# Optimization experiments

Measured on AMD Instinct MI355X. Metric: run time of the kernel, lower is better.

## Reference

```python
import jax, jax.numpy as jnp
import numpy as np

N_NODES = 100000


def _gcn_conv(x, edge_index, W, b, n_nodes):
    """PyG GCNConv: add self-loops, symmetric deg^-1/2 normalization,
    linear transform, scatter-sum aggregation, bias."""
    loop = jnp.arange(n_nodes, dtype=edge_index.dtype)
    src = jnp.concatenate([edge_index[0], loop])  # message sources
    dst = jnp.concatenate([edge_index[1], loop])  # message targets
    deg = jax.ops.segment_sum(jnp.ones_like(dst, dtype=x.dtype), dst,
                              num_segments=n_nodes)
    dinv = jnp.where(deg > 0, jax.lax.rsqrt(jnp.maximum(deg, 1.0)), 0.0)
    norm = dinv[src] * dinv[dst]  # [E+N]
    h = x @ W  # [N, out] transform before aggregation (fewer bytes moved)
    msg = h[src] * norm[:, None]  # [E+N, out]
    out = jax.ops.segment_sum(msg, dst, num_segments=n_nodes)
    return out + b


def setup_inputs() -> dict:
    key = jax.random.key(0)
    k1, k2, k3, k4, k5, k6 = jax.random.split(key, 6)
    in_ch, hid, out_ch = 128, 64, 64
    x = jax.random.normal(k1, (N_NODES, in_ch), dtype=jnp.float32)
    edge_index = jax.random.randint(k2, (2, 3200000), 0, N_NODES, dtype=jnp.int64)
    # Glorot-style init for GCN weights, zeros for bias (PyG default)
    W1 = jax.random.normal(k3, (in_ch, hid), dtype=jnp.float32) / np.sqrt(in_ch)
    b1 = jnp.zeros((hid,), dtype=jnp.float32)
    W2 = jax.random.normal(k4, (hid, out_ch), dtype=jnp.float32) / np.sqrt(hid)
    b2 = jnp.zeros((out_ch,), dtype=jnp.float32)
    return {"x": x, "edge_index": edge_index, "W1": W1, "b1": b1,
            "W2": W2, "b2": b2}


def reference(x, edge_index, W1, b1, W2, b2):
    n = x.shape[0]
    h = _gcn_conv(x, edge_index, W1, b1, n)
    h = jax.nn.relu(h)
    out = _gcn_conv(h, edge_index, W2, b2, n)
    return out
```

## Files before the change

kernel.cpp:

```cpp
#include <hip/hip_runtime.h>
#include <math.h>


#define BKT_SHIFT 9
#define BKT_NODES 512
#define NBSH      256
#define CHUNK     8192
#define MAXB      20480

typedef unsigned short ushort_t;
typedef _Float16 h2_t __attribute__((ext_vector_type(2)));
typedef _Float16 h4_t __attribute__((ext_vector_type(4)));

__global__ __launch_bounds__(256) void bucket_bin(const int* __restrict__ src,
                                                  const int* __restrict__ dst,
                                                  int* __restrict__ bcur,
                                                  unsigned* __restrict__ pairs,
                                                  int E, int NB) {
    __shared__ unsigned stag[CHUNK];
    __shared__ int hist[NBSH];
    __shared__ int lofs[NBSH];
    __shared__ int lcur[NBSH];
    __shared__ int gbase[NBSH];
    const int t  = threadIdx.x;
    const int e0 = blockIdx.x * CHUNK;
    const int n  = min(CHUNK, E - e0);

    for (int i = t; i < NBSH; i += 256) hist[i] = 0;
    __syncthreads();
    for (int i = t; i < n; i += 256) atomicAdd(&hist[dst[e0 + i] >> BKT_SHIFT], 1);
    __syncthreads();
    int v = hist[t];
    lofs[t] = v;
    __syncthreads();
    for (int d = 1; d < 256; d <<= 1) {
        int u = (t >= d) ? lofs[t - d] : 0;
        __syncthreads();
        lofs[t] += u;
        __syncthreads();
    }
    if (t < NB) {
        lcur[t]  = lofs[t] - v;
        gbase[t] = (v > 0) ? t * MAXB + atomicAdd(&bcur[t], v) : 0;
    }
    __syncthreads();
    for (int i = t; i < n; i += 256) {
        int d = dst[e0 + i];
        int s = src[e0 + i];
        int b = d >> BKT_SHIFT;
        int p = atomicAdd(&lcur[b], 1);
        stag[p] = ((unsigned)(d & (BKT_NODES - 1)) << 17) | (unsigned)s;
    }
    __syncthreads();
    const int wv = t >> 6, ln = t & 63;
    for (int b = wv; b < NB; b += 4) {
        int cb = hist[b];
        if (cb == 0) continue;
        int lo = lofs[b] - cb;
        int gb = gbase[b];
        int lim = min(cb, (b + 1) * MAXB - gb);
        for (int i = ln; i < lim; i += 64) pairs[gb + i] = stag[lo + i];
    }
}

__global__ __launch_bounds__(1024) void csr_sort(const unsigned* __restrict__ pairs,
                                                 const int* __restrict__ bcur,
                                                 unsigned* __restrict__ csr,
                                                 int* __restrict__ cnt,
                                                 int* __restrict__ offs,
                                                 float* __restrict__ dinv, int N) {
    extern __shared__ unsigned st[];
    __shared__ int h[BKT_NODES];
    __shared__ int sc[BKT_NODES];
    __shared__ int cur[BKT_NODES];
    const int b    = blockIdx.x;
    const int t    = threadIdx.x;
    const int n0   = b << BKT_SHIFT;
    const int base = b * MAXB;
    const int ne   = min(bcur[b], MAXB);

    if (t < BKT_NODES) h[t] = 0;
    __syncthreads();
    for (int i = t; i < ne; i += 1024) atomicAdd(&h[pairs[base + i] >> 17], 1);
    __syncthreads();
    int v = 0;
    if (t < BKT_NODES) { v = h[t]; sc[t] = v; }
    __syncthreads();
    for (int d = 1; d < BKT_NODES; d <<= 1) {
        int u = (t < BKT_NODES && t >= d) ? sc[t - d] : 0;
        __syncthreads();
        if (t < BKT_NODES) sc[t] += u;
        __syncthreads();
    }
    if (t < BKT_NODES) {
        int ex = sc[t] - v;
        cur[t] = ex;
        int node = n0 + t;
        if (node < N) {
            cnt[node]  = v;
            offs[node] = base + ex;
            dinv[node] = rsqrtf((float)(v + 1));
        }
    }
    __syncthreads();
    for (int i = t; i < ne; i += 1024) {
        unsigned p = pairs[base + i];
        int pos = atomicAdd(&cur[p >> 17], 1);
        st[pos] = p & 0x1FFFFu;
    }
    __syncthreads();
    for (int i = t; i < ne; i += 1024) csr[base + i] = st[i];
}

template <int K>
__global__ __launch_bounds__(256) void gemm_scale(const float* __restrict__ X,
                                                  const float* __restrict__ W,
                                                  const float* __restrict__ dinv,
                                                  ushort_t* __restrict__ G, int N) {
    __shared__ float Ws[K * 64];
    const int t  = threadIdx.x;
    const int r0 = blockIdx.x * 128;

    for (int i = t; i < K * 16; i += 256)
        ((float4*)Ws)[i] = ((const float4*)W)[i];

    const int cg = (t & 15) * 4;
    const int rb = r0 + (t >> 4) * 8;

    float acc[8][4];
#pragma unroll
    for (int j = 0; j < 8; ++j) {
        acc[j][0] = 0.f; acc[j][1] = 0.f; acc[j][2] = 0.f; acc[j][3] = 0.f;
    }
    __syncthreads();

    const bool full = (rb + 8 <= N);
    for (int k = 0; k < K; k += 4) {
        float4 xr[8];
        if (full) {
#pragma unroll
            for (int j = 0; j < 8; ++j)
                xr[j] = *(const float4*)(X + (size_t)(rb + j) * K + k);
        } else {
#pragma unroll
            for (int j = 0; j < 8; ++j)
                xr[j] = (rb + j < N) ? *(const float4*)(X + (size_t)(rb + j) * K + k)
                                     : make_float4(0.f, 0.f, 0.f, 0.f);
        }
#pragma unroll
        for (int kk = 0; kk < 4; ++kk) {
            float4 w = *(const float4*)&Ws[(k + kk) * 64 + cg];
#pragma unroll
            for (int j = 0; j < 8; ++j) {
                float xv = (&xr[j].x)[kk];
                acc[j][0] = fmaf(xv, w.x, acc[j][0]);
                acc[j][1] = fmaf(xv, w.y, acc[j][1]);
                acc[j][2] = fmaf(xv, w.z, acc[j][2]);
                acc[j][3] = fmaf(xv, w.w, acc[j][3]);
            }
        }
    }

#pragma unroll
    for (int j = 0; j < 8; ++j) {
        int row = rb + j;
        if (row < N) {
            float s = dinv[row];
            h4_t o = { (_Float16)(acc[j][0] * s), (_Float16)(acc[j][1] * s),
                       (_Float16)(acc[j][2] * s), (_Float16)(acc[j][3] * s) };
            *(h4_t*)(G + (size_t)row * 64 + cg) = o;
        }
    }
}

#define B2(u) __builtin_bit_cast(h2_t, (u))
#define DOT8(v)                                                          \
    acc[0] = __builtin_amdgcn_fdot2(B2((v).x), selx, acc[0], false);     \
    acc[1] = __builtin_amdgcn_fdot2(B2((v).x), sely, acc[1], false);     \
    acc[2] = __builtin_amdgcn_fdot2(B2((v).y), selx, acc[2], false);     \
    acc[3] = __builtin_amdgcn_fdot2(B2((v).y), sely, acc[3], false);     \
    acc[4] = __builtin_amdgcn_fdot2(B2((v).z), selx, acc[4], false);     \
    acc[5] = __builtin_amdgcn_fdot2(B2((v).z), sely, acc[5], false);     \
    acc[6] = __builtin_amdgcn_fdot2(B2((v).w), selx, acc[6], false);     \
    acc[7] = __builtin_amdgcn_fdot2(B2((v).w), sely, acc[7], false);

__global__ __launch_bounds__(256) void aggregate5(const ushort_t* __restrict__ G,
                                                  const int* __restrict__ offs,
                                                  const int* __restrict__ cnt,
                                                  const unsigned* __restrict__ csr,
                                                  const float* __restrict__ dinv,
                                                  const float* __restrict__ bias,
                                                  float* __restrict__ out, int N,
                                                  int do_relu) {
    int w    = (blockIdx.x * 256 + threadIdx.x) >> 6;
    int lane = threadIdx.x & 63;
    if (w >= N) return;
    const int grp = lane >> 3;
    const int sub = lane & 7;
    const int beg = offs[w];
    const int num = cnt[w];

    const h2_t selx = {(_Float16)1.0f, (_Float16)0.0f};
    const h2_t sely = {(_Float16)0.0f, (_Float16)1.0f};

    float acc[8] = {0.f, 0.f, 0.f, 0.f, 0.f, 0.f, 0.f, 0.f};
    if (grp == 0) {
        uint4 v = *(const uint4*)(G + (size_t)w * 64 + sub * 8);
        DOT8(v);
    }

    int e = 0;
    for (; e + 32 <= num; e += 32) {
        unsigned s0 = csr[beg + e + grp];
        unsigned s1 = csr[beg + e + 8 + grp];
        unsigned s2 = csr[beg + e + 16 + grp];
        unsigned s3 = csr[beg + e + 24 + grp];
        uint4 v0 = *(const uint4*)(G + ((size_t)s0 << 6) + (sub << 3));
        uint4 v1 = *(const uint4*)(G + ((size_t)s1 << 6) + (sub << 3));
        uint4 v2 = *(const uint4*)(G + ((size_t)s2 << 6) + (sub << 3));
        uint4 v3 = *(const uint4*)(G + ((size_t)s3 << 6) + (sub << 3));
        DOT8(v0); DOT8(v1); DOT8(v2); DOT8(v3);
    }
    if (e + 16 <= num) {
        unsigned s0 = csr[beg + e + grp];
        unsigned s1 = csr[beg + e + 8 + grp];
        uint4 v0 = *(const uint4*)(G + ((size_t)s0 << 6) + (sub << 3));
        uint4 v1 = *(const uint4*)(G + ((size_t)s1 << 6) + (sub << 3));
        DOT8(v0); DOT8(v1);
        e += 16;
    }
    if (e + 8 <= num) {
        unsigned s0 = csr[beg + e + grp];
        uint4 v0 = *(const uint4*)(G + ((size_t)s0 << 6) + (sub << 3));
        DOT8(v0);
        e += 8;
    }
    int rem = num - e;
    if (grp < rem) {
        unsigned s0 = csr[beg + e + grp];
        uint4 v0 = *(const uint4*)(G + ((size_t)s0 << 6) + (sub << 3));
        DOT8(v0);
    }

#pragma unroll
    for (int m = 8; m <= 32; m <<= 1) {
#pragma unroll
        for (int j = 0; j < 8; ++j) acc[j] += __shfl_xor(acc[j], m, 64);
    }

    if (grp == 0) {
        float d = dinv[w];
        float4 bl0 = *(const float4*)(bias + sub * 8);
        float4 bl1 = *(const float4*)(bias + sub * 8 + 4);
        float4 o0 = make_float4(fmaf(acc[0], d, bl0.x), fmaf(acc[1], d, bl0.y),
                                fmaf(acc[2], d, bl0.z), fmaf(acc[3], d, bl0.w));
        float4 o1 = make_float4(fmaf(acc[4], d, bl1.x), fmaf(acc[5], d, bl1.y),
                                fmaf(acc[6], d, bl1.z), fmaf(acc[7], d, bl1.w));
        if (do_relu) {
            o0.x = fmaxf(o0.x, 0.f); o0.y = fmaxf(o0.y, 0.f);
            o0.z = fmaxf(o0.z, 0.f); o0.w = fmaxf(o0.w, 0.f);
            o1.x = fmaxf(o1.x, 0.f); o1.y = fmaxf(o1.y, 0.f);
            o1.z = fmaxf(o1.z, 0.f); o1.w = fmaxf(o1.w, 0.f);
        }
        *(float4*)(out + (size_t)w * 64 + sub * 8)     = o0;
        *(float4*)(out + (size_t)w * 64 + sub * 8 + 4) = o1;
    }
}

extern "C" void kernel_launch(void* const* d_in, const int* in_sizes, int n_in,
                              void* d_out, int out_size, void* d_ws, size_t ws_size,
                              hipStream_t stream) {
    const float* x  = (const float*)d_in[0];
    const int*   ei = (const int*)d_in[1];
    const float* W1 = (const float*)d_in[2];
    const float* b1 = (const float*)d_in[3];
    const float* W2 = (const float*)d_in[4];
    const float* b2 = (const float*)d_in[5];
    float* out = (float*)d_out;

    const int IN_CH = 128;
    const int N = in_sizes[0] / IN_CH;
    const int E = in_sizes[1] / 2;
    const int* src = ei;
    const int* dst = ei + E;
    const int NB = (N + BKT_NODES - 1) >> BKT_SHIFT;

    char* ws = (char*)d_ws;
    size_t off = 0;
    auto take = [&](size_t bytes) -> char* {
        char* p = ws + off;
        off += (bytes + 255) & ~(size_t)255;
        return p;
    };
    float*    dinv  = (float*)take((size_t)N * 4);
    int*      cnt   = (int*)take((size_t)N * 4);
    int*      offs  = (int*)take((size_t)N * 4);
    int*      bcur  = (int*)take(NBSH * 4);
    unsigned* csr   = (unsigned*)take(((size_t)NB * MAXB + 64) * 4);
    ushort_t* g     = (ushort_t*)take((size_t)N * 64 * 2);
    float*    a1    = (float*)take((size_t)N * 64 * 4);
    unsigned* pairs = (unsigned*)a1;

    const int nbC = (E + CHUNK - 1) / CHUNK;

    hipMemsetAsync(bcur, 0, NBSH * 4, stream);
    bucket_bin<<<nbC, 256, 0, stream>>>(src, dst, bcur, pairs, E, NB);
    csr_sort<<<NB, 1024, MAXB * 4, stream>>>(pairs, bcur, csr, cnt, offs, dinv, N);

    gemm_scale<128><<<(N + 127) / 128, 256, 0, stream>>>(x, W1, dinv, g, N);
    aggregate5<<<(N + 3) / 4, 256, 0, stream>>>(g, offs, cnt, csr, dinv, b1, a1, N, 1);
    gemm_scale<64><<<(N + 127) / 128, 256, 0, stream>>>(a1, W2, dinv, g, N);
    aggregate5<<<(N + 3) / 4, 256, 0, stream>>>(g, offs, cnt, csr, dinv, b2, out, N, 0);
}
```

Before: 334.8 us.

## Replace bucketed LDS CSR sort with global atomic histogram, scan and scatter

Builds the CSR adjacency with a global per-node histogram using atomics, a three-stage prefix scan, and an atomic scatter of source indices, replacing the two-stage bucket binning and shared-memory sort. Offsets now include a sentinel so the aggregation derives counts from adjacent offsets. This removes the fixed per-bucket capacity and the pairs staging buffer, but relies on millions of contended global atomics and uncoalesced random writes, and adds more kernel launches.

```diff
diff --git a/kernel.cpp b/kernel.cpp
--- a/kernel.cpp
+++ b/kernel.cpp
@@ -1,116 +1,89 @@
 #include <hip/hip_runtime.h>
 #include <math.h>
 
-
-#define BKT_SHIFT 9
-#define BKT_NODES 512
-#define NBSH      256
-#define CHUNK     8192
-#define MAXB      20480
 
 typedef unsigned short ushort_t;
 typedef _Float16 h2_t __attribute__((ext_vector_type(2)));
 typedef _Float16 h4_t __attribute__((ext_vector_type(4)));
 
-__global__ __launch_bounds__(256) void bucket_bin(const int* __restrict__ src,
-                                                  const int* __restrict__ dst,
-                                                  int* __restrict__ bcur,
-                                                  unsigned* __restrict__ pairs,
-                                                  int E, int NB) {
-    __shared__ unsigned stag[CHUNK];
-    __shared__ int hist[NBSH];
-    __shared__ int lofs[NBSH];
-    __shared__ int lcur[NBSH];
-    __shared__ int gbase[NBSH];
-    const int t  = threadIdx.x;
-    const int e0 = blockIdx.x * CHUNK;
-    const int n  = min(CHUNK, E - e0);
-
-    for (int i = t; i < NBSH; i += 256) hist[i] = 0;
-    __syncthreads();
-    for (int i = t; i < n; i += 256) atomicAdd(&hist[dst[e0 + i] >> BKT_SHIFT], 1);
-    __syncthreads();
-    int v = hist[t];
-    lofs[t] = v;
+
+__global__ __launch_bounds__(256) void hist_k(const int* __restrict__ dst,
+                                              int* __restrict__ hist, int E) {
+    int i = blockIdx.x * 256 + threadIdx.x;
+    const int stride = gridDim.x * 256;
+    for (; i < E; i += stride) atomicAdd(&hist[dst[i]], 1);
+}
+
+__global__ __launch_bounds__(256) void scan_blk(const int* __restrict__ hist,
+                                                int* __restrict__ bsum, int N) {
+    __shared__ int sh[256];
+    const int t = threadIdx.x;
+    const int i = blockIdx.x * 256 + t;
+    sh[t] = (i < N) ? hist[i] : 0;
+    __syncthreads();
+    for (int d = 128; d > 0; d >>= 1) {
+        if (t < d) sh[t] += sh[t + d];
+        __syncthreads();
+    }
+    if (t == 0) bsum[blockIdx.x] = sh[0];
+}
+
+__global__ __launch_bounds__(512) void scan_top(const int* __restrict__ bsum,
+                                                int* __restrict__ bbase, int nb) {
+    __shared__ int sh[512];
+    const int t = threadIdx.x;
+    int v = (t < nb) ? bsum[t] : 0;
+    sh[t] = v;
+    __syncthreads();
+    for (int d = 1; d < 512; d <<= 1) {
+        int u = (t >= d) ? sh[t - d] : 0;
+        __syncthreads();
+        sh[t] += u;
+        __syncthreads();
+    }
+    if (t < nb) bbase[t] = sh[t] - v;
+}
+
+__global__ __launch_bounds__(256) void scan_fin(const int* __restrict__ hist,
+                                                const int* __restrict__ bbase,
+                                                int* __restrict__ offs,
+                                                int* __restrict__ cur,
+                                                float* __restrict__ dinv, int N) {
+    __shared__ int sh[256];
+    const int t = threadIdx.x;
+    const int i = blockIdx.x * 256 + t;
+    const int v = (i < N) ? hist[i] : 0;
+    sh[t] = v;
     __syncthreads();
     for (int d = 1; d < 256; d <<= 1) {
-        int u = (t >= d) ? lofs[t - d] : 0;
-        __syncthreads();
-        lofs[t] += u;
-        __syncthreads();
-    }
-    if (t < NB) {
-        lcur[t]  = lofs[t] - v;
-        gbase[t] = (v > 0) ? t * MAXB + atomicAdd(&bcur[t], v) : 0;
-    }
-    __syncthreads();
-    for (int i = t; i < n; i += 256) {
-        int d = dst[e0 + i];
-        int s = src[e0 + i];
-        int b = d >> BKT_SHIFT;
-        int p = atomicAdd(&lcur[b], 1);
-        stag[p] = ((unsigned)(d & (BKT_NODES - 1)) << 17) | (unsigned)s;
-    }
-    __syncthreads();
-    const int wv = t >> 6, ln = t & 63;
-    for (int b = wv; b < NB; b += 4) {
-        int cb = hist[b];
-        if (cb == 0) continue;
-        int lo = lofs[b] - cb;
-        int gb = gbase[b];
-        int lim = min(cb, (b + 1) * MAXB - gb);
-        for (int i = ln; i < lim; i += 64) pairs[gb + i] = stag[lo + i];
-    }
-}
-
-__global__ __launch_bounds__(1024) void csr_sort(const unsigned* __restrict__ pairs,
-                                                 const int* __restrict__ bcur,
-                                                 unsigned* __restrict__ csr,
-                                                 int* __restrict__ cnt,
-                                                 int* __restrict__ offs,
-                                                 float* __restrict__ dinv, int N) {
-    extern __shared__ unsigned st[];
-    __shared__ int h[BKT_NODES];
-    __shared__ int sc[BKT_NODES];
-    __shared__ int cur[BKT_NODES];
-    const int b    = blockIdx.x;
-    const int t    = threadIdx.x;
-    const int n0   = b << BKT_SHIFT;
-    const int base = b * MAXB;
-    const int ne   = min(bcur[b], MAXB);
-
-    if (t < BKT_NODES) h[t] = 0;
-    __syncthreads();
-    for (int i = t; i < ne; i += 1024) atomicAdd(&h[pairs[base + i] >> 17], 1);
-    __syncthreads();
-    int v = 0;
-    if (t < BKT_NODES) { v = h[t]; sc[t] = v; }
-    __syncthreads();
-    for (int d = 1; d < BKT_NODES; d <<= 1) {
-        int u = (t < BKT_NODES && t >= d) ? sc[t - d] : 0;
-        __syncthreads();
-        if (t < BKT_NODES) sc[t] += u;
-        __syncthreads();
-    }
-    if (t < BKT_NODES) {
-        int ex = sc[t] - v;
-        cur[t] = ex;
-        int node = n0 + t;
-        if (node < N) {
-            cnt[node]  = v;
-            offs[node] = base + ex;
-            dinv[node] = rsqrtf((float)(v + 1));
-        }
-    }
-    __syncthreads();
-    for (int i = t; i < ne; i += 1024) {
-        unsigned p = pairs[base + i];
-        int pos = atomicAdd(&cur[p >> 17], 1);
-        st[pos] = p & 0x1FFFFu;
-    }
-    __syncthreads();
-    for (int i = t; i < ne; i += 1024) csr[base + i] = st[i];
-}
+        int u = (t >= d) ? sh[t - d] : 0;
+        __syncthreads();
+        sh[t] += u;
+        __syncthreads();
+    }
+    const int ex = bbase[blockIdx.x] + sh[t] - v;
+    if (i < N) {
+        offs[i] = ex;
+        cur[i]  = ex;
+        dinv[i] = rsqrtf((float)(v + 1));
+        if (i == N - 1) offs[N] = ex + v;
+    }
+}
+
+__global__ __launch_bounds__(256) void scatter_k(const int* __restrict__ src,
+                                                 const int* __restrict__ dst,
+                                                 int* __restrict__ cur,
+                                                 unsigned* __restrict__ csr, int E) {
+    int i = blockIdx.x * 256 + threadIdx.x;
+    const int stride = gridDim.x * 256;
+    for (; i < E; i += stride) {
+        int s = src[i];
+        int d = dst[i];
+        int pos = atomicAdd(&cur[d], 1);
+        csr[pos] = (unsigned)s;
+    }
+}
+
 
 template <int K>
 __global__ __launch_bounds__(256) void gemm_scale(const float* __restrict__ X,
@@ -186,7 +159,6 @@
 
 __global__ __launch_bounds__(256) void aggregate5(const ushort_t* __restrict__ G,
                                                   const int* __restrict__ offs,
-                                                  const int* __restrict__ cnt,
                                                   const unsigned* __restrict__ csr,
                                                   const float* __restrict__ dinv,
                                                   const float* __restrict__ bias,
@@ -198,7 +170,7 @@
     const int grp = lane >> 3;
     const int sub = lane & 7;
     const int beg = offs[w];
-    const int num = cnt[w];
+    const int num = offs[w + 1] - beg;
 
     const h2_t selx = {(_Float16)1.0f, (_Float16)0.0f};
     const h2_t sely = {(_Float16)0.0f, (_Float16)1.0f};
@@ -283,7 +255,7 @@
     const int E = in_sizes[1] / 2;
     const int* src = ei;
     const int* dst = ei + E;
-    const int NB = (N + BKT_NODES - 1) >> BKT_SHIFT;
+    const int NBLK = (N + 255) / 256;
 
     char* ws = (char*)d_ws;
     size_t off = 0;
@@ -293,22 +265,24 @@
         return p;
     };
     float*    dinv  = (float*)take((size_t)N * 4);
-    int*      cnt   = (int*)take((size_t)N * 4);
-    int*      offs  = (int*)take((size_t)N * 4);
-    int*      bcur  = (int*)take(NBSH * 4);
-    unsigned* csr   = (unsigned*)take(((size_t)NB * MAXB + 64) * 4);
+    int*      hist  = (int*)take((size_t)N * 4);
+    int*      offs  = (int*)take(((size_t)N + 1) * 4);
+    int*      cur   = (int*)take((size_t)N * 4);
+    int*      bsum  = (int*)take((size_t)NBLK * 4);
+    int*      bbase = (int*)take((size_t)NBLK * 4);
+    unsigned* csr   = (unsigned*)take((size_t)E * 4);
     ushort_t* g     = (ushort_t*)take((size_t)N * 64 * 2);
     float*    a1    = (float*)take((size_t)N * 64 * 4);
-    unsigned* pairs = (unsigned*)a1;
-
-    const int nbC = (E + CHUNK - 1) / CHUNK;
-
-    hipMemsetAsync(bcur, 0, NBSH * 4, stream);
-    bucket_bin<<<nbC, 256, 0, stream>>>(src, dst, bcur, pairs, E, NB);
-    csr_sort<<<NB, 1024, MAXB * 4, stream>>>(pairs, bcur, csr, cnt, offs, dinv, N);
+
+    (void)hipMemsetAsync(hist, 0, (size_t)N * 4, stream);
+    hist_k<<<2048, 256, 0, stream>>>(dst, hist, E);
+    scan_blk<<<NBLK, 256, 0, stream>>>(hist, bsum, N);
+    scan_top<<<1, 512, 0, stream>>>(bsum, bbase, NBLK);
+    scan_fin<<<NBLK, 256, 0, stream>>>(hist, bbase, offs, cur, dinv, N);
+    scatter_k<<<2048, 256, 0, stream>>>(src, dst, cur, csr, E);
 
     gemm_scale<128><<<(N + 127) / 128, 256, 0, stream>>>(x, W1, dinv, g, N);
-    aggregate5<<<(N + 3) / 4, 256, 0, stream>>>(g, offs, cnt, csr, dinv, b1, a1, N, 1);
+    aggregate5<<<(N + 3) / 4, 256, 0, stream>>>(g, offs, csr, dinv, b1, a1, N, 1);
     gemm_scale<64><<<(N + 127) / 128, 256, 0, stream>>>(a1, W2, dinv, g, N);
-    aggregate5<<<(N + 3) / 4, 256, 0, stream>>>(g, offs, cnt, csr, dinv, b2, out, N, 0);
-}
+    aggregate5<<<(N + 3) / 4, 256, 0, stream>>>(g, offs, csr, dinv, b2, out, N, 0);
+}
```

Measured after the change: 712.5 us. 113% more time.

## Replace FMA-based dense transform with fp16 MFMA matrix-core GEMM

Applied to the files above, without the earlier changes.

The two node-feature transforms (X@W1, A1@W2) now run on MFMA 16x16x32 f16 instructions instead of scalar FP32 FMAs. Inputs and weights are converted to fp16 on the fly, with W transposed into padded shared memory, and the output is scaled by dinv and stored as fp16. This removes the compute cost of the GEMM, which is small next to the memory-bound aggregation. In exchange it lowers input precision to fp16 and writes 2-byte scattered stores per lane instead of vectorized 8-byte stores.

```diff
diff --git a/kernel.cpp b/kernel.cpp
--- a/kernel.cpp
+++ b/kernel.cpp
@@ -10,7 +10,8 @@
 
 typedef unsigned short ushort_t;
 typedef _Float16 h2_t __attribute__((ext_vector_type(2)));
-typedef _Float16 h4_t __attribute__((ext_vector_type(4)));
+typedef _Float16 h8_t __attribute__((ext_vector_type(8)));
+typedef float    f4_t __attribute__((ext_vector_type(4)));
 
 __global__ __launch_bounds__(256) void bucket_bin(const int* __restrict__ src,
                                                   const int* __restrict__ dst,
@@ -113,62 +114,63 @@
 }
 
 template <int K>
-__global__ __launch_bounds__(256) void gemm_scale(const float* __restrict__ X,
-                                                  const float* __restrict__ W,
-                                                  const float* __restrict__ dinv,
-                                                  ushort_t* __restrict__ G, int N) {
-    __shared__ float Ws[K * 64];
+__global__ __launch_bounds__(256) void gemm_mfma(const float* __restrict__ X,
+                                                 const float* __restrict__ W,
+                                                 const float* __restrict__ dinv,
+                                                 ushort_t* __restrict__ G, int N) {
+    __shared__ _Float16 Wt[64][K + 8];
     const int t  = threadIdx.x;
-    const int r0 = blockIdx.x * 128;
-
-    for (int i = t; i < K * 16; i += 256)
-        ((float4*)Ws)[i] = ((const float4*)W)[i];
-
-    const int cg = (t & 15) * 4;
-    const int rb = r0 + (t >> 4) * 8;
-
-    float acc[8][4];
-#pragma unroll
-    for (int j = 0; j < 8; ++j) {
-        acc[j][0] = 0.f; acc[j][1] = 0.f; acc[j][2] = 0.f; acc[j][3] = 0.f;
-    }
-    __syncthreads();
-
-    const bool full = (rb + 8 <= N);
-    for (int k = 0; k < K; k += 4) {
-        float4 xr[8];
-        if (full) {
-#pragma unroll
-            for (int j = 0; j < 8; ++j)
-                xr[j] = *(const float4*)(X + (size_t)(rb + j) * K + k);
+    const int wv = t >> 6, ln = t & 63;
+    const int rbase = blockIdx.x * 64 + wv * 16;
+
+    for (int i = t; i < K * 16; i += 256) {
+        int k  = i >> 4;
+        int c4 = (i & 15) * 4;
+        float4 w = ((const float4*)W)[i];
+        Wt[c4 + 0][k] = (_Float16)w.x;
+        Wt[c4 + 1][k] = (_Float16)w.y;
+        Wt[c4 + 2][k] = (_Float16)w.z;
+        Wt[c4 + 3][k] = (_Float16)w.w;
+    }
+    __syncthreads();
+
+    const int row  = rbase + (ln & 15);
+    const int kgrp = (ln >> 4) * 8;
+    const bool rok = (row < N);
+
+    f4_t acc[4];
+#pragma unroll
+    for (int c = 0; c < 4; ++c) acc[c] = (f4_t){0.f, 0.f, 0.f, 0.f};
+
+    for (int kk = 0; kk < K; kk += 32) {
+        h8_t a;
+        if (rok) {
+            float4 x0 = *(const float4*)(X + (size_t)row * K + kk + kgrp);
+            float4 x1 = *(const float4*)(X + (size_t)row * K + kk + kgrp + 4);
+            a[0] = (_Float16)x0.x; a[1] = (_Float16)x0.y;
+            a[2] = (_Float16)x0.z; a[3] = (_Float16)x0.w;
+            a[4] = (_Float16)x1.x; a[5] = (_Float16)x1.y;
+            a[6] = (_Float16)x1.z; a[7] = (_Float16)x1.w;
         } else {
 #pragma unroll
-            for (int j = 0; j < 8; ++j)
-                xr[j] = (rb + j < N) ? *(const float4*)(X + (size_t)(rb + j) * K + k)
-                                     : make_float4(0.f, 0.f, 0.f, 0.f);
-        }
-#pragma unroll
-        for (int kk = 0; kk < 4; ++kk) {
-            float4 w = *(const float4*)&Ws[(k + kk) * 64 + cg];
-#pragma unroll
-            for (int j = 0; j < 8; ++j) {
-                float xv = (&xr[j].x)[kk];
-                acc[j][0] = fmaf(xv, w.x, acc[j][0]);
-                acc[j][1] = fmaf(xv, w.y, acc[j][1]);
-                acc[j][2] = fmaf(xv, w.z, acc[j][2]);
-                acc[j][3] = fmaf(xv, w.w, acc[j][3]);
-            }
-        }
-    }
-
-#pragma unroll
-    for (int j = 0; j < 8; ++j) {
-        int row = rb + j;
-        if (row < N) {
-            float s = dinv[row];
-            h4_t o = { (_Float16)(acc[j][0] * s), (_Float16)(acc[j][1] * s),
-                       (_Float16)(acc[j][2] * s), (_Float16)(acc[j][3] * s) };
-            *(h4_t*)(G + (size_t)row * 64 + cg) = o;
+            for (int j = 0; j < 8; ++j) a[j] = (_Float16)0.0f;
+        }
+#pragma unroll
+        for (int c = 0; c < 4; ++c) {
+            h8_t b = *(const h8_t*)&Wt[c * 16 + (ln & 15)][kk + kgrp];
+            acc[c] = __builtin_amdgcn_mfma_f32_16x16x32_f16(a, b, acc[c], 0, 0, 0);
+        }
+    }
+
+    _Float16* Gh = (_Float16*)G;
+#pragma unroll
+    for (int r = 0; r < 4; ++r) {
+        int rn = rbase + ((ln >> 4) << 2) + r;
+        if (rn < N) {
+            float dv = dinv[rn];
+#pragma unroll
+            for (int c = 0; c < 4; ++c)
+                Gh[(size_t)rn * 64 + c * 16 + (ln & 15)] = (_Float16)(acc[c][r] * dv);
         }
     }
 }
@@ -302,13 +304,14 @@
     unsigned* pairs = (unsigned*)a1;
 
     const int nbC = (E + CHUNK - 1) / CHUNK;
-
-    hipMemsetAsync(bcur, 0, NBSH * 4, stream);
+    const int nbG = (N + 63) / 64;
+
+    (void)hipMemsetAsync(bcur, 0, NBSH * 4, stream);
     bucket_bin<<<nbC, 256, 0, stream>>>(src, dst, bcur, pairs, E, NB);
     csr_sort<<<NB, 1024, MAXB * 4, stream>>>(pairs, bcur, csr, cnt, offs, dinv, N);
 
-    gemm_scale<128><<<(N + 127) / 128, 256, 0, stream>>>(x, W1, dinv, g, N);
+    gemm_mfma<128><<<nbG, 256, 0, stream>>>(x, W1, dinv, g, N);
     aggregate5<<<(N + 3) / 4, 256, 0, stream>>>(g, offs, cnt, csr, dinv, b1, a1, N, 1);
-    gemm_scale<64><<<(N + 127) / 128, 256, 0, stream>>>(a1, W2, dinv, g, N);
+    gemm_mfma<64><<<nbG, 256, 0, stream>>>(a1, W2, dinv, g, N);
     aggregate5<<<(N + 3) / 4, 256, 0, stream>>>(g, offs, cnt, csr, dinv, b2, out, N, 0);
 }
```

Result: faster. 295.2 us (-11.8%).
